# Kernel tuning notes

Hardware: AMD Instinct MI355X
Metric: run time of the kernel (lower is better)

Reference implementation:

```python
import jax, jax.numpy as jnp
import numpy as np


def setup_inputs() -> dict:
    key = jax.random.key(0)
    kx, kw = jax.random.split(key)
    x = jax.random.normal(kx, (32, 256, 56, 56), dtype=jnp.float32)
    weight = jax.random.uniform(kw, (256, 256, 3, 3), dtype=jnp.float32) * 0.001
    return {"x": x, "weight": weight}


def reference(x, weight):
    # --- binarize activations with straight-through estimator ---
    # forward value = sign(x); gradient flows through clamp(x, -1, 1)
    clipped_x = jnp.clip(x, -1.0, 1.0)
    bx = jax.lax.stop_gradient(jnp.sign(x) - clipped_x) + clipped_x

    # --- binarize weights (per-output-channel mean-centered, scaled sign) ---
    w = weight
    # subtract per-output-channel mean over (in_c, kh, kw)
    bw = w - jnp.mean(w.reshape(w.shape[0], -1), axis=-1)[:, None, None, None]
    # per-output-channel scaling factor = mean |bw| (detached)
    scale = jnp.mean(jnp.abs(bw), axis=(1, 2, 3), keepdims=True)
    scale = jax.lax.stop_gradient(scale)
    clipped_w = jnp.clip(bw, -1.0, 1.0)
    binary_w = jax.lax.stop_gradient(scale * jnp.sign(bw) - clipped_w) + clipped_w

    # --- conv2d, NCHW / OIHW, stride 1, padding 1 ---
    y = jax.lax.conv_general_dilated(
        bx, binary_w,
        window_strides=(1, 1),
        padding=((1, 1), (1, 1)),
        dimension_numbers=("NCHW", "OIHW", "NCHW"),
    )
    return y
```

## Files before the change

kernel.cpp:

```cpp
#include <hip/hip_runtime.h>
#include <cstdint>
#include <cstddef>

#define N_ 32
#define C_ 256
#define H_ 56
#define W_ 56

typedef int v4i __attribute__((ext_vector_type(4)));
typedef uint32_t __attribute__((address_space(1))) glb_u32;
typedef uint32_t __attribute__((address_space(3))) lds_u32;

static constexpr size_t SX_BYTES = (size_t)N_ * 58 * 68 * 256;
static constexpr size_t WB_OFF   = SX_BYTES;
static constexpr size_t WB_BYTES = 36ull * 16 * 64 * 16;
static constexpr size_t SC_OFF   = WB_OFF + WB_BYTES;

__device__ __forceinline__ uint32_t sgnw(uint32_t u) {
    return (u & 0x7fffffffu) ? (((uint32_t)(((int)u) >> 31) | 1u) & 0xffu) : 0u;
}

__global__ __launch_bounds__(256) void pack_x(const float* __restrict__ x,
                                              char* __restrict__ sx) {
    int tid = threadIdx.x;
    int n   = blockIdx.y;
    v4i z = {0, 0, 0, 0};

    if (blockIdx.x >= 49) {
        if (blockIdx.x == 49) {
            for (int i = tid; i < 2 * 58 * 16; i += 256) {
                int r   = i / (58 * 16);
                int rem = i - r * (58 * 16);
                char* base = sx + ((size_t)n * 58 + (size_t)r * 57) * (68 * 256);
                *(v4i*)(base + (size_t)rem * 16) = z;
            }
        } else {
            for (int i = tid; i < 56 * 32; i += 256) {
                int r = 1 + (i >> 5);
                int c = i & 31;
                int wpos = (c >> 4) * 57, ch = c & 15;
                *(v4i*)(sx + (((size_t)n * 58 + r) * 68 + wpos) * 256 + ch * 16) = z;
            }
        }
        return;
    }

    __shared__ char ob[64 * 256];
    int hw0 = blockIdx.x * 64;

    int ch  = tid >> 4;
    int hw4 = tid & 15;

    const float* xb = x + ((size_t)n * C_ + ch * 16) * 3136 + hw0 + hw4 * 4;

    uint32_t t[4][4];
#pragma unroll
    for (int p = 0; p < 4; ++p) {
        uint32_t w0, w1, w2, w3;
        {
            float4 v = *(const float4*)(xb + (size_t)(4 * p + 0) * 3136);
            w0 = sgnw(__float_as_uint(v.x)) | (sgnw(__float_as_uint(v.y)) << 8) |
                 (sgnw(__float_as_uint(v.z)) << 16) | (sgnw(__float_as_uint(v.w)) << 24);
        }
        {
            float4 v = *(const float4*)(xb + (size_t)(4 * p + 1) * 3136);
            w1 = sgnw(__float_as_uint(v.x)) | (sgnw(__float_as_uint(v.y)) << 8) |
                 (sgnw(__float_as_uint(v.z)) << 16) | (sgnw(__float_as_uint(v.w)) << 24);
        }
        {
            float4 v = *(const float4*)(xb + (size_t)(4 * p + 2) * 3136);
            w2 = sgnw(__float_as_uint(v.x)) | (sgnw(__float_as_uint(v.y)) << 8) |
                 (sgnw(__float_as_uint(v.z)) << 16) | (sgnw(__float_as_uint(v.w)) << 24);
        }
        {
            float4 v = *(const float4*)(xb + (size_t)(4 * p + 3) * 3136);
            w3 = sgnw(__float_as_uint(v.x)) | (sgnw(__float_as_uint(v.y)) << 8) |
                 (sgnw(__float_as_uint(v.z)) << 16) | (sgnw(__float_as_uint(v.w)) << 24);
        }
        uint32_t lo01 = __builtin_amdgcn_perm(w1, w0, 0x05010400u);
        uint32_t hi01 = __builtin_amdgcn_perm(w1, w0, 0x07030602u);
        uint32_t lo23 = __builtin_amdgcn_perm(w3, w2, 0x05010400u);
        uint32_t hi23 = __builtin_amdgcn_perm(w3, w2, 0x07030602u);
        t[p][0] = __builtin_amdgcn_perm(lo23, lo01, 0x05040100u);
        t[p][1] = __builtin_amdgcn_perm(lo23, lo01, 0x07060302u);
        t[p][2] = __builtin_amdgcn_perm(hi23, hi01, 0x05040100u);
        t[p][3] = __builtin_amdgcn_perm(hi23, hi01, 0x07060302u);
    }

#pragma unroll
    for (int h = 0; h < 4; ++h) {
        int row  = hw4 * 4 + h;
        int slot = (ch + row) & 15;
        v4i c4 = {(int)t[0][h], (int)t[1][h], (int)t[2][h], (int)t[3][h]};
        *(v4i*)(ob + row * 256 + slot * 16) = c4;
    }
    __syncthreads();

#pragma unroll
    for (int j = 0; j < 4; ++j) {
        int i = tid + j * 256;
        int hwl3 = i >> 4, cc = i & 15;
        v4i v = *(const v4i*)(ob + hwl3 * 256 + ((cc + hwl3) & 15) * 16);
        int hw = hw0 + hwl3;
        int h = hw / 56, w = hw - h * 56;
        int slot = (cc + (w + 1)) & 15;
        *(v4i*)(sx + (((size_t)n * 58 + h + 1) * 68 + (w + 1)) * 256 + slot * 16) = v;
    }
}

__global__ __launch_bounds__(256) void pack_w(const float* __restrict__ wt,
                                              char* __restrict__ wB,
                                              float* __restrict__ scaleg) {
    __shared__ double red[256];
    int o = blockIdx.x, tid = threadIdx.x;
    const float* wo = wt + (size_t)o * 2304;

    double s = 0;
    for (int j = tid; j < 2304; j += 256) s += (double)wo[j];
    red[tid] = s;
    __syncthreads();
    for (int k = 128; k > 0; k >>= 1) {
        if (tid < k) red[tid] += red[tid + k];
        __syncthreads();
    }
    double mean = red[0] / 2304.0;
    __syncthreads();

    double s2 = 0;
    for (int j = tid; j < 2304; j += 256) s2 += fabs((double)wo[j] - mean);
    red[tid] = s2;
    __syncthreads();
    for (int k = 128; k > 0; k >>= 1) {
        if (tid < k) red[tid] += red[tid + k];
        __syncthreads();
    }
    if (tid == 0) scaleg[o] = (float)(red[0] / 2304.0);

    if (tid < 144) {
        int kiter = tid >> 2, q = tid & 3;
        int tap = kiter >> 2, cb = kiter & 3;
        int kh = tap / 3, kw = tap - kh * 3;
        int words[4];
        for (int g = 0; g < 4; ++g) {
            int word = 0;
            for (int b = 0; b < 4; ++b) {
                int c = cb * 64 + q * 16 + g * 4 + b;
                double v = (double)wo[c * 9 + kh * 3 + kw];
                int sg = (v > mean) - (v < mean);
                word |= (sg & 0xff) << (8 * b);
            }
            words[g] = word;
        }
        v4i pk = {words[0], words[1], words[2], words[3]};
        *(v4i*)(wB + (((size_t)kiter * 16 + (o >> 4)) * 64 + q * 16 + (o & 15)) * 16) = pk;
    }
}

__device__ __forceinline__ void stage_chunk(const char* src, char* xs, int i) {
    int pos = i >> 4;
    int row = (pos * 1130) >> 16;
    int w   = pos - row * 58;
    const char* g = src + (((size_t)(row * 68 + w)) << 8) + ((size_t)(i & 15) << 4);
    char* l = xs + (size_t)i * 16;
    __builtin_amdgcn_global_load_lds((const glb_u32*)g, (lds_u32*)l, 16, 0, 0);
}

__global__ __launch_bounds__(512, 2) void conv_mfma(const char* __restrict__ sx,
                                                    const v4i* __restrict__ wB,
                                                    const float* __restrict__ scaleg,
                                                    float* __restrict__ out) {
    __shared__ char xs[6 * 58 * 256];
    int tid = threadIdx.x;
    int wave = tid >> 6, lane = tid & 63;
    int hq = blockIdx.x, n = blockIdx.y;
    int h0 = hq * 4;

    const char* src = sx + ((size_t)n * 58 + h0) * (68 * 256);
#pragma unroll
    for (int it = 0; it < 10; ++it) stage_chunk(src, xs, tid + it * 512);
    if (tid < 448) stage_chunk(src, xs, tid + 5120);

    int lm = lane & 15, q = lane >> 4;
    int og = wave & 3, mg = wave >> 2;
    int kstart = __builtin_amdgcn_readfirstlane((9 * wave) >> 1);

    int posb[7], slotb[7];
#pragma unroll
    for (int mf = 0; mf < 7; ++mf) {
        int m = mg * 112 + mf * 16 + lm;
        int r = m / 56;
        int wof = m - r * 56;
        posb[mf]  = r * 58 + wof;
        slotb[mf] = q + wof;
    }

    v4i acc[7][4];
#pragma unroll
    for (int mf = 0; mf < 7; ++mf)
#pragma unroll
        for (int of = 0; of < 4; ++of) { v4i z = {0, 0, 0, 0}; acc[mf][of] = z; }

    const v4i* wBw = wB + (size_t)(og * 4) * 64 + lane;

    auto wrap = [&](int t) { int k = kstart + t; return k >= 36 ? k - 36 : k; };
    auto loadB = [&](int k, v4i (&b)[4]) {
#pragma unroll
        for (int of = 0; of < 4; ++of) b[of] = wBw[(size_t)k * 1024 + of * 64];
    };

    __syncthreads();

    v4i bR0[4], bR1[4], bR2[4];
    loadB(wrap(0), bR0);
    loadB(wrap(1), bR1);
    loadB(wrap(2), bR2);

    auto step = [&](v4i (&bReg)[4], int t) {
        int k = wrap(t);
        int tap = k >> 2, cb = k & 3;
        int dh = (tap * 11) >> 5;
        int dw = tap - dh * 3;
        int pofs = dh * 58 + dw;
        int sofs = cb * 4 + dw;
        v4i a[7];
#pragma unroll
        for (int mf = 0; mf < 7; ++mf) {
            int pos  = posb[mf] + pofs;
            int slot = (slotb[mf] + sofs) & 15;
            a[mf] = *(const v4i*)(xs + ((size_t)pos << 8) + ((size_t)slot << 4));
        }
        __builtin_amdgcn_s_setprio(1);
#pragma unroll
        for (int mf = 0; mf < 7; ++mf)
#pragma unroll
            for (int of = 0; of < 4; ++of)
                acc[mf][of] = __builtin_amdgcn_mfma_i32_16x16x64_i8(
                    a[mf], bReg[of], acc[mf][of], 0, 0, 0);
        __builtin_amdgcn_s_setprio(0);
        loadB(wrap(t + 3), bReg);
    };

    for (int t3 = 0; t3 < 12; ++t3) {
        int t = t3 * 3;
        step(bR0, t);
        step(bR1, t + 1);
        step(bR2, t + 2);
    }

#pragma unroll
    for (int of = 0; of < 4; ++of) {
        int o = og * 64 + of * 16 + lm;
        float s = scaleg[o];
#pragma unroll
        for (int mf = 0; mf < 7; ++mf) {
            int m  = mg * 112 + mf * 16 + q * 4;
            int r  = m / 56;
            int wb = m - r * 56;
            float* ob = out + ((size_t)(n * C_ + o) * H_ + h0 + r) * W_ + wb;
            float4 v = {s * (float)acc[mf][of].x, s * (float)acc[mf][of].y,
                        s * (float)acc[mf][of].z, s * (float)acc[mf][of].w};
            *(float4*)ob = v;
        }
    }
}

extern "C" void kernel_launch(void* const* d_in, const int* in_sizes, int n_in,
                              void* d_out, int out_size, void* d_ws, size_t ws_size,
                              hipStream_t stream) {
    const float* x   = (const float*)d_in[0];
    const float* wgt = (const float*)d_in[1];
    float* out = (float*)d_out;
    char* ws = (char*)d_ws;

    char*  sx = ws;
    char*  wb = ws + WB_OFF;
    float* sg = (float*)(ws + SC_OFF);

    pack_x<<<dim3(51, N_), dim3(256), 0, stream>>>(x, sx);
    pack_w<<<dim3(256), dim3(256), 0, stream>>>(wgt, wb, sg);
    conv_mfma<<<dim3(14, N_), dim3(512), 0, stream>>>(sx, (const v4i*)wb, sg, out);
}
```

Measured before the change: 251.9 us.

## Fuse weight packing into pack_x and add producer wave to overlap staging with conv

Weight binarization now runs as extra blocks of the activation-packing kernel, which removes one kernel launch. The conv kernel now handles 8 output rows per block using 576 threads. A dedicated ninth wave stages the next 4 rows into LDS while the eight compute waves process the first 4 rows. In exchange, LDS grows to 10 row-slabs, occupancy drops to one block per CU, and the grid shrinks to 224 blocks, which could leave CUs underused.

Result: slower. 582.1 us (+131.1%).

```diff
diff --git a/kernel.cpp b/kernel.cpp
--- a/kernel.cpp
+++ b/kernel.cpp
@@ -20,12 +20,67 @@
     return (u & 0x7fffffffu) ? (((uint32_t)(((int)u) >> 31) | 1u) & 0xffu) : 0u;
 }
 
+__device__ void pack_w_body(const float* __restrict__ wt,
+                            char* __restrict__ wB,
+                            float* __restrict__ scaleg, int o) {
+    __shared__ double red[256];
+    int tid = threadIdx.x;
+    const float* wo = wt + (size_t)o * 2304;
+
+    double s = 0;
+    for (int j = tid; j < 2304; j += 256) s += (double)wo[j];
+    red[tid] = s;
+    __syncthreads();
+    for (int k = 128; k > 0; k >>= 1) {
+        if (tid < k) red[tid] += red[tid + k];
+        __syncthreads();
+    }
+    double mean = red[0] / 2304.0;
+    __syncthreads();
+
+    double s2 = 0;
+    for (int j = tid; j < 2304; j += 256) s2 += fabs((double)wo[j] - mean);
+    red[tid] = s2;
+    __syncthreads();
+    for (int k = 128; k > 0; k >>= 1) {
+        if (tid < k) red[tid] += red[tid + k];
+        __syncthreads();
+    }
+    if (tid == 0) scaleg[o] = (float)(red[0] / 2304.0);
+
+    if (tid < 144) {
+        int kiter = tid >> 2, q = tid & 3;
+        int tap = kiter >> 2, cb = kiter & 3;
+        int kh = tap / 3, kw = tap - kh * 3;
+        int words[4];
+        for (int g = 0; g < 4; ++g) {
+            int word = 0;
+            for (int b = 0; b < 4; ++b) {
+                int c = cb * 64 + q * 16 + g * 4 + b;
+                double v = (double)wo[c * 9 + kh * 3 + kw];
+                int sg = (v > mean) - (v < mean);
+                word |= (sg & 0xff) << (8 * b);
+            }
+            words[g] = word;
+        }
+        v4i pk = {words[0], words[1], words[2], words[3]};
+        *(v4i*)(wB + (((size_t)kiter * 16 + (o >> 4)) * 64 + q * 16 + (o & 15)) * 16) = pk;
+    }
+}
+
 __global__ __launch_bounds__(256) void pack_x(const float* __restrict__ x,
-                                              char* __restrict__ sx) {
+                                              char* __restrict__ sx,
+                                              const float* __restrict__ wt,
+                                              char* __restrict__ wB,
+                                              float* __restrict__ scaleg) {
     int tid = threadIdx.x;
     int n   = blockIdx.y;
     v4i z = {0, 0, 0, 0};
 
+    if (blockIdx.x >= 51) {
+        pack_w_body(wt, wB, scaleg, (blockIdx.x - 51) * 32 + n);
+        return;
+    }
     if (blockIdx.x >= 49) {
         if (blockIdx.x == 49) {
             for (int i = tid; i < 2 * 58 * 16; i += 256) {
@@ -108,54 +163,6 @@
     }
 }
 
-__global__ __launch_bounds__(256) void pack_w(const float* __restrict__ wt,
-                                              char* __restrict__ wB,
-                                              float* __restrict__ scaleg) {
-    __shared__ double red[256];
-    int o = blockIdx.x, tid = threadIdx.x;
-    const float* wo = wt + (size_t)o * 2304;
-
-    double s = 0;
-    for (int j = tid; j < 2304; j += 256) s += (double)wo[j];
-    red[tid] = s;
-    __syncthreads();
-    for (int k = 128; k > 0; k >>= 1) {
-        if (tid < k) red[tid] += red[tid + k];
-        __syncthreads();
-    }
-    double mean = red[0] / 2304.0;
-    __syncthreads();
-
-    double s2 = 0;
-    for (int j = tid; j < 2304; j += 256) s2 += fabs((double)wo[j] - mean);
-    red[tid] = s2;
-    __syncthreads();
-    for (int k = 128; k > 0; k >>= 1) {
-        if (tid < k) red[tid] += red[tid + k];
-        __syncthreads();
-    }
-    if (tid == 0) scaleg[o] = (float)(red[0] / 2304.0);
-
-    if (tid < 144) {
-        int kiter = tid >> 2, q = tid & 3;
-        int tap = kiter >> 2, cb = kiter & 3;
-        int kh = tap / 3, kw = tap - kh * 3;
-        int words[4];
-        for (int g = 0; g < 4; ++g) {
-            int word = 0;
-            for (int b = 0; b < 4; ++b) {
-                int c = cb * 64 + q * 16 + g * 4 + b;
-                double v = (double)wo[c * 9 + kh * 3 + kw];
-                int sg = (v > mean) - (v < mean);
-                word |= (sg & 0xff) << (8 * b);
-            }
-            words[g] = word;
-        }
-        v4i pk = {words[0], words[1], words[2], words[3]};
-        *(v4i*)(wB + (((size_t)kiter * 16 + (o >> 4)) * 64 + q * 16 + (o & 15)) * 16) = pk;
-    }
-}
-
 __device__ __forceinline__ void stage_chunk(const char* src, char* xs, int i) {
     int pos = i >> 4;
     int row = (pos * 1130) >> 16;
@@ -165,21 +172,11 @@
     __builtin_amdgcn_global_load_lds((const glb_u32*)g, (lds_u32*)l, 16, 0, 0);
 }
 
-__global__ __launch_bounds__(512, 2) void conv_mfma(const char* __restrict__ sx,
-                                                    const v4i* __restrict__ wB,
-                                                    const float* __restrict__ scaleg,
-                                                    float* __restrict__ out) {
-    __shared__ char xs[6 * 58 * 256];
-    int tid = threadIdx.x;
-    int wave = tid >> 6, lane = tid & 63;
-    int hq = blockIdx.x, n = blockIdx.y;
-    int h0 = hq * 4;
-
-    const char* src = sx + ((size_t)n * 58 + h0) * (68 * 256);
-#pragma unroll
-    for (int it = 0; it < 10; ++it) stage_chunk(src, xs, tid + it * 512);
-    if (tid < 448) stage_chunk(src, xs, tid + 5120);
-
+__device__ __forceinline__ void conv_tile(const char* __restrict__ xs,
+                                          const v4i* __restrict__ wB,
+                                          const float* __restrict__ scaleg,
+                                          float* __restrict__ out,
+                                          int wave, int lane, int n, int h0) {
     int lm = lane & 15, q = lane >> 4;
     int og = wave & 3, mg = wave >> 2;
     int kstart = __builtin_amdgcn_readfirstlane((9 * wave) >> 1);
@@ -207,8 +204,6 @@
 #pragma unroll
         for (int of = 0; of < 4; ++of) b[of] = wBw[(size_t)k * 1024 + of * 64];
     };
-
-    __syncthreads();
 
     v4i bR0[4], bR1[4], bR2[4];
     loadB(wrap(0), bR0);
@@ -264,6 +259,36 @@
     }
 }
 
+__global__ __launch_bounds__(576, 1) void conv_mfma(const char* __restrict__ sx,
+                                                    const v4i* __restrict__ wB,
+                                                    const float* __restrict__ scaleg,
+                                                    float* __restrict__ out) {
+    __shared__ char xs[10 * 58 * 256];
+    int tid = threadIdx.x;
+    int wave = tid >> 6, lane = tid & 63;
+    int j = blockIdx.x, n = blockIdx.y;
+    int h0 = j * 8;
+
+    const char* src = sx + ((size_t)n * 58 + h0) * (68 * 256);
+
+    if (wave == 8) {
+        for (int i = lane; i < 6 * 58 * 16; i += 64) stage_chunk(src, xs, i);
+    }
+    __syncthreads();
+
+    if (wave == 8) {
+        const char* s2 = src + (size_t)6 * 68 * 256;
+        char* x2 = xs + (size_t)6 * 58 * 256;
+        for (int i = lane; i < 4 * 58 * 16; i += 64) stage_chunk(s2, x2, i);
+    } else {
+        conv_tile(xs, wB, scaleg, out, wave, lane, n, h0);
+    }
+    __syncthreads();
+
+    if (wave < 8)
+        conv_tile(xs + (size_t)4 * 58 * 256, wB, scaleg, out, wave, lane, n, h0 + 4);
+}
+
 extern "C" void kernel_launch(void* const* d_in, const int* in_sizes, int n_in,
                               void* d_out, int out_size, void* d_ws, size_t ws_size,
                               hipStream_t stream) {
@@ -276,7 +301,6 @@
     char*  wb = ws + WB_OFF;
     float* sg = (float*)(ws + SC_OFF);
 
-    pack_x<<<dim3(51, N_), dim3(256), 0, stream>>>(x, sx);
-    pack_w<<<dim3(256), dim3(256), 0, stream>>>(wgt, wb, sg);
-    conv_mfma<<<dim3(14, N_), dim3(512), 0, stream>>>(sx, (const v4i*)wb, sg, out);
-}
+    pack_x<<<dim3(59, N_), dim3(256), 0, stream>>>(x, sx, wgt, wb, sg);
+    conv_mfma<<<dim3(7, N_), dim3(576), 0, stream>>>(sx, (const v4i*)wb, sg, out);
+}
```

## Merge weight packing into pack_x launch and double-buffer conv main loop with barriers

Applied to the files above, without the earlier changes.

The weight-packing kernel becomes extra blocks of the activation-packing kernel, which removes one kernel launch and lets both packing jobs run concurrently. The conv main loop drops the staggered per-wave k-start rotation and the triple-buffered B registers. In their place it uses explicit ping-pong A/B register buffers, prefetching the next k step's LDS and global operands while the current MFMAs run, with s_barrier calls to keep waves in lockstep. The barriers add synchronisation cost and may cause all waves to contend for LDS at the same time, where the old staggered start spread that access out.

After: 265.6 us. 1.05x slower.

```diff
diff --git a/kernel.cpp b/kernel.cpp
--- a/kernel.cpp
+++ b/kernel.cpp
@@ -20,12 +20,67 @@
     return (u & 0x7fffffffu) ? (((uint32_t)(((int)u) >> 31) | 1u) & 0xffu) : 0u;
 }
 
+__device__ void pack_w_body(const float* __restrict__ wt,
+                            char* __restrict__ wB,
+                            float* __restrict__ scaleg, int o) {
+    __shared__ double red[256];
+    int tid = threadIdx.x;
+    const float* wo = wt + (size_t)o * 2304;
+
+    double s = 0;
+    for (int j = tid; j < 2304; j += 256) s += (double)wo[j];
+    red[tid] = s;
+    __syncthreads();
+    for (int k = 128; k > 0; k >>= 1) {
+        if (tid < k) red[tid] += red[tid + k];
+        __syncthreads();
+    }
+    double mean = red[0] / 2304.0;
+    __syncthreads();
+
+    double s2 = 0;
+    for (int j = tid; j < 2304; j += 256) s2 += fabs((double)wo[j] - mean);
+    red[tid] = s2;
+    __syncthreads();
+    for (int k = 128; k > 0; k >>= 1) {
+        if (tid < k) red[tid] += red[tid + k];
+        __syncthreads();
+    }
+    if (tid == 0) scaleg[o] = (float)(red[0] / 2304.0);
+
+    if (tid < 144) {
+        int kiter = tid >> 2, q = tid & 3;
+        int tap = kiter >> 2, cb = kiter & 3;
+        int kh = tap / 3, kw = tap - kh * 3;
+        int words[4];
+        for (int g = 0; g < 4; ++g) {
+            int word = 0;
+            for (int b = 0; b < 4; ++b) {
+                int c = cb * 64 + q * 16 + g * 4 + b;
+                double v = (double)wo[c * 9 + kh * 3 + kw];
+                int sg = (v > mean) - (v < mean);
+                word |= (sg & 0xff) << (8 * b);
+            }
+            words[g] = word;
+        }
+        v4i pk = {words[0], words[1], words[2], words[3]};
+        *(v4i*)(wB + (((size_t)kiter * 16 + (o >> 4)) * 64 + q * 16 + (o & 15)) * 16) = pk;
+    }
+}
+
 __global__ __launch_bounds__(256) void pack_x(const float* __restrict__ x,
-                                              char* __restrict__ sx) {
+                                              char* __restrict__ sx,
+                                              const float* __restrict__ wt,
+                                              char* __restrict__ wB,
+                                              float* __restrict__ scaleg) {
     int tid = threadIdx.x;
     int n   = blockIdx.y;
     v4i z = {0, 0, 0, 0};
 
+    if (blockIdx.x >= 51) {
+        pack_w_body(wt, wB, scaleg, (blockIdx.x - 51) * 32 + n);
+        return;
+    }
     if (blockIdx.x >= 49) {
         if (blockIdx.x == 49) {
             for (int i = tid; i < 2 * 58 * 16; i += 256) {
@@ -108,54 +163,6 @@
     }
 }
 
-__global__ __launch_bounds__(256) void pack_w(const float* __restrict__ wt,
-                                              char* __restrict__ wB,
-                                              float* __restrict__ scaleg) {
-    __shared__ double red[256];
-    int o = blockIdx.x, tid = threadIdx.x;
-    const float* wo = wt + (size_t)o * 2304;
-
-    double s = 0;
-    for (int j = tid; j < 2304; j += 256) s += (double)wo[j];
-    red[tid] = s;
-    __syncthreads();
-    for (int k = 128; k > 0; k >>= 1) {
-        if (tid < k) red[tid] += red[tid + k];
-        __syncthreads();
-    }
-    double mean = red[0] / 2304.0;
-    __syncthreads();
-
-    double s2 = 0;
-    for (int j = tid; j < 2304; j += 256) s2 += fabs((double)wo[j] - mean);
-    red[tid] = s2;
-    __syncthreads();
-    for (int k = 128; k > 0; k >>= 1) {
-        if (tid < k) red[tid] += red[tid + k];
-        __syncthreads();
-    }
-    if (tid == 0) scaleg[o] = (float)(red[0] / 2304.0);
-
-    if (tid < 144) {
-        int kiter = tid >> 2, q = tid & 3;
-        int tap = kiter >> 2, cb = kiter & 3;
-        int kh = tap / 3, kw = tap - kh * 3;
-        int words[4];
-        for (int g = 0; g < 4; ++g) {
-            int word = 0;
-            for (int b = 0; b < 4; ++b) {
-                int c = cb * 64 + q * 16 + g * 4 + b;
-                double v = (double)wo[c * 9 + kh * 3 + kw];
-                int sg = (v > mean) - (v < mean);
-                word |= (sg & 0xff) << (8 * b);
-            }
-            words[g] = word;
-        }
-        v4i pk = {words[0], words[1], words[2], words[3]};
-        *(v4i*)(wB + (((size_t)kiter * 16 + (o >> 4)) * 64 + q * 16 + (o & 15)) * 16) = pk;
-    }
-}
-
 __device__ __forceinline__ void stage_chunk(const char* src, char* xs, int i) {
     int pos = i >> 4;
     int row = (pos * 1130) >> 16;
@@ -182,7 +189,6 @@
 
     int lm = lane & 15, q = lane >> 4;
     int og = wave & 3, mg = wave >> 2;
-    int kstart = __builtin_amdgcn_readfirstlane((9 * wave) >> 1);
 
     int posb[7], slotb[7];
 #pragma unroll
@@ -202,49 +208,58 @@
 
     const v4i* wBw = wB + (size_t)(og * 4) * 64 + lane;
 
-    auto wrap = [&](int t) { int k = kstart + t; return k >= 36 ? k - 36 : k; };
     auto loadB = [&](int k, v4i (&b)[4]) {
 #pragma unroll
         for (int of = 0; of < 4; ++of) b[of] = wBw[(size_t)k * 1024 + of * 64];
     };
-
-    __syncthreads();
-
-    v4i bR0[4], bR1[4], bR2[4];
-    loadB(wrap(0), bR0);
-    loadB(wrap(1), bR1);
-    loadB(wrap(2), bR2);
-
-    auto step = [&](v4i (&bReg)[4], int t) {
-        int k = wrap(t);
+    auto loadA = [&](int k, v4i (&a)[7]) {
         int tap = k >> 2, cb = k & 3;
         int dh = (tap * 11) >> 5;
         int dw = tap - dh * 3;
         int pofs = dh * 58 + dw;
         int sofs = cb * 4 + dw;
-        v4i a[7];
 #pragma unroll
         for (int mf = 0; mf < 7; ++mf) {
             int pos  = posb[mf] + pofs;
             int slot = (slotb[mf] + sofs) & 15;
             a[mf] = *(const v4i*)(xs + ((size_t)pos << 8) + ((size_t)slot << 4));
         }
+    };
+
+    __syncthreads();
+
+    v4i aA[7], aB[7], bA[4], bB[4];
+    loadB(0, bA);
+    loadA(0, aA);
+
+    for (int t2 = 0; t2 < 18; ++t2) {
+        int ke = 2 * t2;
+        int ko = ke + 1;
+        int kn = (ke + 2 >= 36) ? 0 : ke + 2;
+        loadB(ko, bB);
+        loadA(ko, aB);
+        __builtin_amdgcn_s_barrier();
         __builtin_amdgcn_s_setprio(1);
 #pragma unroll
         for (int mf = 0; mf < 7; ++mf)
 #pragma unroll
             for (int of = 0; of < 4; ++of)
                 acc[mf][of] = __builtin_amdgcn_mfma_i32_16x16x64_i8(
-                    a[mf], bReg[of], acc[mf][of], 0, 0, 0);
+                    aA[mf], bA[of], acc[mf][of], 0, 0, 0);
         __builtin_amdgcn_s_setprio(0);
-        loadB(wrap(t + 3), bReg);
-    };
-
-    for (int t3 = 0; t3 < 12; ++t3) {
-        int t = t3 * 3;
-        step(bR0, t);
-        step(bR1, t + 1);
-        step(bR2, t + 2);
+        __builtin_amdgcn_s_barrier();
+        loadB(kn, bA);
+        loadA(kn, aA);
+        __builtin_amdgcn_s_barrier();
+        __builtin_amdgcn_s_setprio(1);
+#pragma unroll
+        for (int mf = 0; mf < 7; ++mf)
+#pragma unroll
+            for (int of = 0; of < 4; ++of)
+                acc[mf][of] = __builtin_amdgcn_mfma_i32_16x16x64_i8(
+                    aB[mf], bB[of], acc[mf][of], 0, 0, 0);
+        __builtin_amdgcn_s_setprio(0);
+        __builtin_amdgcn_s_barrier();
     }
 
 #pragma unroll
@@ -276,7 +291,6 @@
     char*  wb = ws + WB_OFF;
     float* sg = (float*)(ws + SC_OFF);
 
-    pack_x<<<dim3(51, N_), dim3(256), 0, stream>>>(x, sx);
-    pack_w<<<dim3(256), dim3(256), 0, stream>>>(wgt, wb, sg);
+    pack_x<<<dim3(59, N_), dim3(256), 0, stream>>>(x, sx, wgt, wb, sg);
     conv_mfma<<<dim3(14, N_), dim3(512), 0, stream>>>(sx, (const v4i*)wb, sg, out);
 }
```

## Fuse activation binarization and packing into the conv kernel's LDS staging

Applied to the files above, without the earlier changes.

Removes the separate pack_x kernel and its padded int8 intermediate buffer in global memory. Each conv block now reads the float input rows it needs (4 output rows plus halo), takes their sign, transposes channel bytes with perm, and writes the packed tile straight into LDS. Halo columns and out-of-range rows are zero-filled in LDS. This saves a launch and the write and re-read of the intermediate. In exchange, halo rows of x are read about 1.5 times, and the asynchronous global-to-LDS copies become synchronous loads plus ALU work ahead of the MFMA loop.

Result: faster. 246.9 us (-2.0%).

```diff
diff --git a/kernel.cpp b/kernel.cpp
--- a/kernel.cpp
+++ b/kernel.cpp
@@ -8,104 +8,12 @@
 #define W_ 56
 
 typedef int v4i __attribute__((ext_vector_type(4)));
-typedef uint32_t __attribute__((address_space(1))) glb_u32;
-typedef uint32_t __attribute__((address_space(3))) lds_u32;
-
-static constexpr size_t SX_BYTES = (size_t)N_ * 58 * 68 * 256;
-static constexpr size_t WB_OFF   = SX_BYTES;
+
 static constexpr size_t WB_BYTES = 36ull * 16 * 64 * 16;
-static constexpr size_t SC_OFF   = WB_OFF + WB_BYTES;
+static constexpr size_t SC_OFF   = WB_BYTES;
 
 __device__ __forceinline__ uint32_t sgnw(uint32_t u) {
     return (u & 0x7fffffffu) ? (((uint32_t)(((int)u) >> 31) | 1u) & 0xffu) : 0u;
-}
-
-__global__ __launch_bounds__(256) void pack_x(const float* __restrict__ x,
-                                              char* __restrict__ sx) {
-    int tid = threadIdx.x;
-    int n   = blockIdx.y;
-    v4i z = {0, 0, 0, 0};
-
-    if (blockIdx.x >= 49) {
-        if (blockIdx.x == 49) {
-            for (int i = tid; i < 2 * 58 * 16; i += 256) {
-                int r   = i / (58 * 16);
-                int rem = i - r * (58 * 16);
-                char* base = sx + ((size_t)n * 58 + (size_t)r * 57) * (68 * 256);
-                *(v4i*)(base + (size_t)rem * 16) = z;
-            }
-        } else {
-            for (int i = tid; i < 56 * 32; i += 256) {
-                int r = 1 + (i >> 5);
-                int c = i & 31;
-                int wpos = (c >> 4) * 57, ch = c & 15;
-                *(v4i*)(sx + (((size_t)n * 58 + r) * 68 + wpos) * 256 + ch * 16) = z;
-            }
-        }
-        return;
-    }
-
-    __shared__ char ob[64 * 256];
-    int hw0 = blockIdx.x * 64;
-
-    int ch  = tid >> 4;
-    int hw4 = tid & 15;
-
-    const float* xb = x + ((size_t)n * C_ + ch * 16) * 3136 + hw0 + hw4 * 4;
-
-    uint32_t t[4][4];
-#pragma unroll
-    for (int p = 0; p < 4; ++p) {
-        uint32_t w0, w1, w2, w3;
-        {
-            float4 v = *(const float4*)(xb + (size_t)(4 * p + 0) * 3136);
-            w0 = sgnw(__float_as_uint(v.x)) | (sgnw(__float_as_uint(v.y)) << 8) |
-                 (sgnw(__float_as_uint(v.z)) << 16) | (sgnw(__float_as_uint(v.w)) << 24);
-        }
-        {
-            float4 v = *(const float4*)(xb + (size_t)(4 * p + 1) * 3136);
-            w1 = sgnw(__float_as_uint(v.x)) | (sgnw(__float_as_uint(v.y)) << 8) |
-                 (sgnw(__float_as_uint(v.z)) << 16) | (sgnw(__float_as_uint(v.w)) << 24);
-        }
-        {
-            float4 v = *(const float4*)(xb + (size_t)(4 * p + 2) * 3136);
-            w2 = sgnw(__float_as_uint(v.x)) | (sgnw(__float_as_uint(v.y)) << 8) |
-                 (sgnw(__float_as_uint(v.z)) << 16) | (sgnw(__float_as_uint(v.w)) << 24);
-        }
-        {
-            float4 v = *(const float4*)(xb + (size_t)(4 * p + 3) * 3136);
-            w3 = sgnw(__float_as_uint(v.x)) | (sgnw(__float_as_uint(v.y)) << 8) |
-                 (sgnw(__float_as_uint(v.z)) << 16) | (sgnw(__float_as_uint(v.w)) << 24);
-        }
-        uint32_t lo01 = __builtin_amdgcn_perm(w1, w0, 0x05010400u);
-        uint32_t hi01 = __builtin_amdgcn_perm(w1, w0, 0x07030602u);
-        uint32_t lo23 = __builtin_amdgcn_perm(w3, w2, 0x05010400u);
-        uint32_t hi23 = __builtin_amdgcn_perm(w3, w2, 0x07030602u);
-        t[p][0] = __builtin_amdgcn_perm(lo23, lo01, 0x05040100u);
-        t[p][1] = __builtin_amdgcn_perm(lo23, lo01, 0x07060302u);
-        t[p][2] = __builtin_amdgcn_perm(hi23, hi01, 0x05040100u);
-        t[p][3] = __builtin_amdgcn_perm(hi23, hi01, 0x07060302u);
-    }
-
-#pragma unroll
-    for (int h = 0; h < 4; ++h) {
-        int row  = hw4 * 4 + h;
-        int slot = (ch + row) & 15;
-        v4i c4 = {(int)t[0][h], (int)t[1][h], (int)t[2][h], (int)t[3][h]};
-        *(v4i*)(ob + row * 256 + slot * 16) = c4;
-    }
-    __syncthreads();
-
-#pragma unroll
-    for (int j = 0; j < 4; ++j) {
-        int i = tid + j * 256;
-        int hwl3 = i >> 4, cc = i & 15;
-        v4i v = *(const v4i*)(ob + hwl3 * 256 + ((cc + hwl3) & 15) * 16);
-        int hw = hw0 + hwl3;
-        int h = hw / 56, w = hw - h * 56;
-        int slot = (cc + (w + 1)) & 15;
-        *(v4i*)(sx + (((size_t)n * 58 + h + 1) * 68 + (w + 1)) * 256 + slot * 16) = v;
-    }
 }
 
 __global__ __launch_bounds__(256) void pack_w(const float* __restrict__ wt,
@@ -156,16 +64,7 @@
     }
 }
 
-__device__ __forceinline__ void stage_chunk(const char* src, char* xs, int i) {
-    int pos = i >> 4;
-    int row = (pos * 1130) >> 16;
-    int w   = pos - row * 58;
-    const char* g = src + (((size_t)(row * 68 + w)) << 8) + ((size_t)(i & 15) << 4);
-    char* l = xs + (size_t)i * 16;
-    __builtin_amdgcn_global_load_lds((const glb_u32*)g, (lds_u32*)l, 16, 0, 0);
-}
-
-__global__ __launch_bounds__(512, 2) void conv_mfma(const char* __restrict__ sx,
+__global__ __launch_bounds__(512, 2) void conv_mfma(const float* __restrict__ x,
                                                     const v4i* __restrict__ wB,
                                                     const float* __restrict__ scaleg,
                                                     float* __restrict__ out) {
@@ -175,10 +74,73 @@
     int hq = blockIdx.x, n = blockIdx.y;
     int h0 = hq * 4;
 
-    const char* src = sx + ((size_t)n * 58 + h0) * (68 * 256);
-#pragma unroll
-    for (int it = 0; it < 10; ++it) stage_chunk(src, xs, tid + it * 512);
-    if (tid < 448) stage_chunk(src, xs, tid + 5120);
+    if (tid < 192) {
+        int r  = tid >> 5;
+        int c2 = tid & 31;
+        int wp = (c2 >> 4) * 57;
+        int ch = c2 & 15;
+        int slot = (ch + wp) & 15;
+        v4i z = {0, 0, 0, 0};
+        *(v4i*)(xs + ((size_t)(r * 58 + wp) << 8) + (slot << 4)) = z;
+    }
+    for (int u = tid; u < 6 * 16 * 14; u += 512) {
+        int R   = u / 224;
+        int rem = u - R * 224;
+        int ch  = rem / 14;
+        int wq  = rem - ch * 14;
+        int ir  = h0 + R - 1;
+        if (ir < 0 || ir > 55) {
+            v4i z = {0, 0, 0, 0};
+#pragma unroll
+            for (int h = 0; h < 4; ++h) {
+                int wp = 1 + wq * 4 + h;
+                int slot = (ch + wp) & 15;
+                *(v4i*)(xs + ((size_t)(R * 58 + wp) << 8) + (slot << 4)) = z;
+            }
+            continue;
+        }
+        const float* xb = x + ((size_t)n * C_ + ch * 16) * 3136 + ir * 56 + wq * 4;
+        uint32_t t[4][4];
+#pragma unroll
+        for (int p = 0; p < 4; ++p) {
+            uint32_t w0, w1, w2, w3;
+            {
+                float4 v = *(const float4*)(xb + (size_t)(4 * p + 0) * 3136);
+                w0 = sgnw(__float_as_uint(v.x)) | (sgnw(__float_as_uint(v.y)) << 8) |
+                     (sgnw(__float_as_uint(v.z)) << 16) | (sgnw(__float_as_uint(v.w)) << 24);
+            }
+            {
+                float4 v = *(const float4*)(xb + (size_t)(4 * p + 1) * 3136);
+                w1 = sgnw(__float_as_uint(v.x)) | (sgnw(__float_as_uint(v.y)) << 8) |
+                     (sgnw(__float_as_uint(v.z)) << 16) | (sgnw(__float_as_uint(v.w)) << 24);
+            }
+            {
+                float4 v = *(const float4*)(xb + (size_t)(4 * p + 2) * 3136);
+                w2 = sgnw(__float_as_uint(v.x)) | (sgnw(__float_as_uint(v.y)) << 8) |
+                     (sgnw(__float_as_uint(v.z)) << 16) | (sgnw(__float_as_uint(v.w)) << 24);
+            }
+            {
+                float4 v = *(const float4*)(xb + (size_t)(4 * p + 3) * 3136);
+                w3 = sgnw(__float_as_uint(v.x)) | (sgnw(__float_as_uint(v.y)) << 8) |
+                     (sgnw(__float_as_uint(v.z)) << 16) | (sgnw(__float_as_uint(v.w)) << 24);
+            }
+            uint32_t lo01 = __builtin_amdgcn_perm(w1, w0, 0x05010400u);
+            uint32_t hi01 = __builtin_amdgcn_perm(w1, w0, 0x07030602u);
+            uint32_t lo23 = __builtin_amdgcn_perm(w3, w2, 0x05010400u);
+            uint32_t hi23 = __builtin_amdgcn_perm(w3, w2, 0x07030602u);
+            t[p][0] = __builtin_amdgcn_perm(lo23, lo01, 0x05040100u);
+            t[p][1] = __builtin_amdgcn_perm(lo23, lo01, 0x07060302u);
+            t[p][2] = __builtin_amdgcn_perm(hi23, hi01, 0x05040100u);
+            t[p][3] = __builtin_amdgcn_perm(hi23, hi01, 0x07060302u);
+        }
+#pragma unroll
+        for (int h = 0; h < 4; ++h) {
+            int wp = 1 + wq * 4 + h;
+            int slot = (ch + wp) & 15;
+            v4i c4 = {(int)t[0][h], (int)t[1][h], (int)t[2][h], (int)t[3][h]};
+            *(v4i*)(xs + ((size_t)(R * 58 + wp) << 8) + (slot << 4)) = c4;
+        }
+    }
 
     int lm = lane & 15, q = lane >> 4;
     int og = wave & 3, mg = wave >> 2;
@@ -272,11 +234,9 @@
     float* out = (float*)d_out;
     char* ws = (char*)d_ws;
 
-    char*  sx = ws;
-    char*  wb = ws + WB_OFF;
+    char*  wb = ws;
     float* sg = (float*)(ws + SC_OFF);
 
-    pack_x<<<dim3(51, N_), dim3(256), 0, stream>>>(x, sx);
     pack_w<<<dim3(256), dim3(256), 0, stream>>>(wgt, wb, sg);
-    conv_mfma<<<dim3(14, N_), dim3(512), 0, stream>>>(sx, (const v4i*)wb, sg, out);
-}
+    conv_mfma<<<dim3(14, N_), dim3(512), 0, stream>>>(x, (const v4i*)wb, sg, out);
+}
```
